# Performance work log

Measured on AMD Instinct MI355X. Metric: run time of the kernel, lower is better.

Reference implementation:

```python
import jax, jax.numpy as jnp
import numpy as np

B = 16
NT, NH_, NW_, T_, H_, W_ = 4, 14, 14, 4, 1, 1
C = 768
NHEAD = 12
HD = C // NHEAD
SCALE = 1.0 / float(np.sqrt(HD))
TT = NT * T_            # 16 temporal slices
T2 = TT // 2            # 8 after even/odd split
HW = (NH_ * H_) * (NW_ * W_)  # 196 spatial tokens
TOKENS = NT * NH_ * NW_ * T_ * H_ * W_


def setup_inputs() -> dict:
    key = jax.random.key(0)
    ks = jax.random.split(key, 14)
    def lin(k, din, dout):
        return jax.random.normal(k, (din, dout), jnp.float32) * 0.02
    return {
        "x_in": jax.random.normal(ks[0], (B, TOKENS, C), jnp.float32),
        "Wq_d": lin(ks[1], C, C),      "bq_d": jnp.zeros((C,), jnp.float32),
        "Wkv_a": lin(ks[2], C, 2 * C), "bkv_a": jnp.zeros((2 * C,), jnp.float32),
        "Wq_a": lin(ks[3], C, C),      "bq_a": jnp.zeros((C,), jnp.float32),
        "Wkv_d": lin(ks[4], C, 2 * C), "bkv_d": jnp.zeros((2 * C,), jnp.float32),
        "Wp_d": lin(ks[5], C, C),      "bp_d": jnp.zeros((C,), jnp.float32),
        "Wp_a": lin(ks[6], C, C),      "bp_a": jnp.zeros((C,), jnp.float32),
    }


def _cross_attn(q_x, kv_x, Wq, bq, Wkv, bkv):
    # q_x, kv_x: (b, t, hw, c)
    b, t, hw, c = q_x.shape
    q = (q_x @ Wq + bq).reshape(b, t, hw, NHEAD, HD)
    kv = (kv_x @ Wkv + bkv).reshape(b, t, hw, 2, NHEAD, HD)
    k, v = kv[..., 0, :, :], kv[..., 1, :, :]
    s = jnp.einsum('btqhd,btkhd->bthqk', q, k) * SCALE
    p = jax.nn.softmax(s, axis=-1)
    o = jnp.einsum('bthqk,btkhd->btqhd', p, v)
    return o.reshape(b, t, hw, c)


def reference(x_in, Wq_d, bq_d, Wkv_a, bkv_a, Wq_a, bq_a, Wkv_d, bkv_d,
              Wp_d, bp_d, Wp_a, bp_a):
    b = x_in.shape[0]
    # einops: b (nt nh nw t h w) c -> b (nt t) (nh h) (nw w) c
    x = x_in.reshape(b, NT, NH_, NW_, T_, H_, W_, C)
    x = x.transpose(0, 1, 4, 2, 5, 3, 6, 7).reshape(b, TT, NH_ * H_, NW_ * W_, C)
    x_skip = x                                   # (b, TT, h, w, c)
    x = x.reshape(b, TT, HW, C)                  # (b, TT, hw, c)
    x_a = x[:, 0::2]                             # (b, T2, hw, c) approx
    x_d = x[:, 1::2]                             # (b, T2, hw, c) detail

    # detail cross-attends to approx, subtract-update
    _d = _cross_attn(x_d, x_a, Wq_d, bq_d, Wkv_a, bkv_a)
    _d = jax.nn.gelu(_d @ Wp_d + bp_d, approximate=False)
    x_d = x_d - _d
    # approx cross-attends to updated detail, add-update
    _a = _cross_attn(x_a, x_d, Wq_a, bq_a, Wkv_d, bkv_d)
    _a = jax.nn.gelu(_a @ Wp_a + bp_a, approximate=False)
    x_a = x_a + _a

    # relaxed_constrain: pooled-skip minus channel-mean of x_a
    xs = x_skip.reshape(b, TT, HW, C)
    pooled = xs.reshape(b, T2, 2, HW, C).mean(axis=2)   # avg_pool2d (2,1)
    pool_a = pooled.mean(axis=-1) - x_a.mean(axis=-1)   # (b, T2, hw)

    # SSL=False: mean over channels, keepdim (torch layout b,1,t,hw)
    x_d_out = x_d.mean(axis=-1)[:, None, :, :]          # (b, 1, T2, hw)
    return (pool_a, x_d_out)
```

## Files before the change

### kernel.cpp

```cpp
#include <hip/hip_runtime.h>

typedef __bf16 bf16;
typedef __attribute__((ext_vector_type(8))) __bf16 bf16x8;
typedef __attribute__((ext_vector_type(4))) __bf16 bf16x4;
typedef __attribute__((ext_vector_type(2))) __bf16 bf16x2;
typedef __attribute__((ext_vector_type(4))) float f32x4;
typedef __attribute__((ext_vector_type(4))) unsigned int u32x4;

#define TOKENS 3136
#define CC 768
#define S196 196
#define M_ROWS 25088
#define BATCH 16

__device__ __forceinline__ float bf2f(bf16 x) { return (float)x; }
__device__ __forceinline__ bf16 f2bf(float x) { return (bf16)x; }

__device__ __forceinline__ float gelu_exact(float x) {
    return 0.5f * x * (1.0f + erff(x * 0.70710678118654752f));
}

__device__ __forceinline__ unsigned int packbf(float a, float b) {
    bf16x2 v; v[0] = (bf16)a; v[1] = (bf16)b;
    return __builtin_bit_cast(unsigned int, v);
}

#define GLOAD_LDS16(gp, lp) \
    __builtin_amdgcn_global_load_lds((const __attribute__((address_space(1))) void*)(gp), \
                                     (__attribute__((address_space(3))) void*)(lp), 16, 0, 0)

__global__ __launch_bounds__(256)
void transpose_all(const float* W0, const float* W1, const float* W2,
                   const float* W3, const float* W4, const float* W5,
                   bf16* D0, bf16* D1, bf16* D2, bf16* D3, bf16* D4, bf16* D5)
{
    const int base[7] = {0, 576, 1728, 2304, 3456, 4032, 4608};
    const float* srcs[6] = {W0, W1, W2, W3, W4, W5};
    bf16*        dsts[6] = {D0, D1, D2, D3, D4, D5};
    const int    Ns[6]   = {768, 1536, 768, 1536, 768, 768};

    int bid = blockIdx.x;
    int which = 0;
    #pragma unroll
    for (int j = 0; j < 6; ++j) if (bid >= base[j + 1]) which = j + 1;
    int t  = bid - base[which];
    int N  = Ns[which];
    const float* W  = srcs[which];
    bf16*        Wt = dsts[which];
    const int K = 768;

    int kx = t % 24, ny = t / 24;
    int k0 = kx * 32, n0 = ny * 32;

    __shared__ float tle[32][33];
    int tx = threadIdx.x & 31, ty = threadIdx.x >> 5;
    for (int r = ty; r < 32; r += 8)
        tle[r][tx] = W[(long)(k0 + r) * N + n0 + tx];
    __syncthreads();
    for (int r = ty; r < 32; r += 8)
        Wt[(long)(n0 + r) * K + k0 + tx] = f2bf(tle[tx][r]);
}

__global__ __launch_bounds__(256)
void conv_bias(const float* b0, const float* b1, const float* b2,
               const float* b3, const float* b4, const float* b5,
               bf16* __restrict__ dst)
{
    const float* srcs[6] = {b0, b1, b2, b3, b4, b5};
    const int sizes[6]   = {768, 1536, 768, 1536, 768, 768};
    const int offs[6]    = {0, 768, 2304, 3072, 4608, 5376};
    int which = blockIdx.x;
    const float* s = srcs[which];
    int n = sizes[which];
    bf16* d = dst + offs[which];
    for (int i = threadIdx.x; i < n; i += 256)
        d[i] = f2bf(s[i]);
}

__global__ __launch_bounds__(256)
void reorder_split(const float* __restrict__ x_in, bf16* __restrict__ xa,
                   bf16* __restrict__ xd)
{
    long idx = (long)blockIdx.x * 256 + threadIdx.x;
    const long total = (long)BATCH * 16 * S196 * 96;
    if (idx >= total) return;
    int  c8  = (int)(idx % 96) * 8;
    long row = idx / 96;
    int  s   = (int)(row % S196);
    long r2  = row / S196;
    int  tt  = (int)(r2 & 15);
    int  b   = (int)(r2 >> 4);
    int  nt  = tt >> 2, t = tt & 3;
    int  nh  = s / 14,  nw = s % 14;
    long src  = ((long)b * TOKENS + ((nt * 14 + nh) * 14 + nw) * 4 + t) * CC + c8;
    bf16* dst = (tt & 1) ? xd : xa;
    long doff = ((long)(b * 8 + (tt >> 1)) * S196 + s) * CC + c8;
    const float* sp = x_in + src;
    f32x4 a = *(const f32x4*)sp;
    f32x4 c = *(const f32x4*)(sp + 4);
    bf16x8 v;
    v[0] = f2bf(a[0]); v[1] = f2bf(a[1]); v[2] = f2bf(a[2]); v[3] = f2bf(a[3]);
    v[4] = f2bf(c[0]); v[5] = f2bf(c[1]); v[6] = f2bf(c[2]); v[7] = f2bf(c[3]);
    *(bf16x8*)(dst + doff) = v;
}

__device__ __forceinline__ float row_sum768(const bf16* __restrict__ p, int lane)
{
    float s = 0.f;
    bf16x8 v = *(const bf16x8*)(p + lane * 8);
    #pragma unroll
    for (int j = 0; j < 8; ++j) s += bf2f(v[j]);
    if (lane < 32) {
        bf16x8 w = *(const bf16x8*)(p + 512 + lane * 8);
        #pragma unroll
        for (int j = 0; j < 8; ++j) s += bf2f(w[j]);
    }
    #pragma unroll
    for (int off = 32; off; off >>= 1) s += __shfl_xor(s, off, 64);
    return s;
}

__global__ __launch_bounds__(256)
void pool_ad(const bf16* __restrict__ xa, const bf16* __restrict__ xd,
             float* __restrict__ pool0, float* __restrict__ rs_a,
             float* __restrict__ rs_d)
{
    int id = blockIdx.x * 4 + (threadIdx.x >> 6);
    int lane = threadIdx.x & 63;
    float sa = row_sum768(xa + (long)id * CC, lane);
    float sd = row_sum768(xd + (long)id * CC, lane);
    if (lane == 0) {
        pool0[id] = (sa + sd) * (0.5f / 768.0f);
        rs_a[id] = 0.f;
        rs_d[id] = 0.f;
    }
}

__global__ __launch_bounds__(256)
void out_combine(const float* __restrict__ pool0, const float* __restrict__ rs_a,
                 const float* __restrict__ rs_d, float* __restrict__ out)
{
    int id = blockIdx.x * 256 + threadIdx.x;
    if (id < M_ROWS) {
        out[id]          = pool0[id] - rs_a[id] * (1.0f / 768.0f);
        out[M_ROWS + id] = rs_d[id] * (1.0f / 768.0f);
    }
}

template<int EPI>
__global__ __launch_bounds__(256, 4)
void gemm_bt128(const bf16* __restrict__ A, const bf16* __restrict__ Bt,
                const bf16* __restrict__ bias, const bf16* __restrict__ res,
                bf16* __restrict__ C, float* __restrict__ rowsum,
                int ldc, int K, int mTiles, int nTiles)
{
    constexpr int BM = 128, BK = 32;
    __shared__ alignas(16) bf16 sA[BM * BK];
    __shared__ alignas(16) bf16 sB[BM * BK];
    const int tid  = threadIdx.x;
    const int lane = tid & 63, wave = tid >> 6;
    const int wm   = wave >> 1, wn = wave & 1;
    const int quad = lane >> 4, l16 = lane & 15;

    int nwg  = (int)gridDim.x;
    int orig = (int)blockIdx.x;
    int q8 = nwg >> 3, r8 = nwg & 7, xcd = orig & 7;
    int pid = (xcd < r8 ? xcd * (q8 + 1) : r8 * (q8 + 1) + (xcd - r8) * q8)
              + (orig >> 3);

    const int GM = 16;
    int group = GM * nTiles;
    int gid   = pid / group;
    int rem   = pid - gid * group;
    int first = gid * GM;
    int gm    = (mTiles - first < GM) ? (mTiles - first) : GM;
    int bm    = first + rem % gm;
    int bn    = rem / gm;

    const long m0 = (long)bm * BM;
    const long n0 = (long)bn * BM;

    f32x4 acc[4][4] = {};

    for (int kt = 0; kt < K; kt += BK) {
        if (kt) __syncthreads();
        #pragma unroll
        for (int c = 0; c < 2; ++c) {
            int ci = (wave * 2 + c) * 64 + lane;
            int r  = ci >> 2, kc = ci & 3;
            const bf16* ga = A  + (m0 + r) * K + kt + kc * 8;
            const bf16* gb = Bt + (n0 + r) * K + kt + kc * 8;
            bf16* la = sA + (wave * 2 + c) * 512;
            bf16* lb = sB + (wave * 2 + c) * 512;
            GLOAD_LDS16(ga, la);
            GLOAD_LDS16(gb, lb);
        }
        __syncthreads();

        bf16x8 af[4], bfr[4];
        #pragma unroll
        for (int mi = 0; mi < 4; ++mi)
            af[mi] = *(const bf16x8*)(sA + (wm * 64 + mi * 16 + l16) * BK + quad * 8);
        #pragma unroll
        for (int ni = 0; ni < 4; ++ni)
            bfr[ni] = *(const bf16x8*)(sB + (wn * 64 + ni * 16 + l16) * BK + quad * 8);
        #pragma unroll
        for (int mi = 0; mi < 4; ++mi)
            #pragma unroll
            for (int ni = 0; ni < 4; ++ni)
                acc[mi][ni] = __builtin_amdgcn_mfma_f32_16x16x32_bf16(af[mi], bfr[ni], acc[mi][ni], 0, 0, 0);
    }

    float bns[4];
    #pragma unroll
    for (int ni = 0; ni < 4; ++ni)
        bns[ni] = bf2f(bias[(int)n0 + wn * 64 + ni * 16 + l16]);

    #pragma unroll
    for (int mi = 0; mi < 4; ++mi) {
        float rs[4] = {0.f, 0.f, 0.f, 0.f};
        int mg = (int)m0 + wm * 64 + mi * 16 + quad * 4;
        #pragma unroll
        for (int ni = 0; ni < 4; ++ni) {
            int ng = (int)n0 + wn * 64 + ni * 16 + l16;
            #pragma unroll
            for (int r = 0; r < 4; ++r) {
                float x = acc[mi][ni][r] + bns[ni];
                long off = (long)(mg + r) * ldc + ng;
                if (EPI == 0) {
                    C[off] = f2bf(x);
                } else if (EPI == 1) {
                    bf16 v = f2bf(bf2f(res[off]) - gelu_exact(x));
                    C[off] = v;
                    rs[r] += bf2f(v);
                } else {
                    bf16 v = f2bf(bf2f(res[off]) + gelu_exact(x));
                    rs[r] += bf2f(v);
                }
            }
        }
        if (EPI != 0) {
            #pragma unroll
            for (int r = 0; r < 4; ++r) {
                float v = rs[r];
                v += __shfl_xor(v, 1, 64);
                v += __shfl_xor(v, 2, 64);
                v += __shfl_xor(v, 4, 64);
                v += __shfl_xor(v, 8, 64);
                if (l16 == 0)
                    atomicAdd(&rowsum[mg + r], v);
            }
        }
    }
}

template<int EPI>
__global__ __launch_bounds__(512, 2)
void gemm_bt256(const bf16* __restrict__ A, const bf16* __restrict__ Bt,
                const bf16* __restrict__ bias, const bf16* __restrict__ res,
                bf16* __restrict__ C, int ldc, int mTiles, int nTiles)
{
    constexpr int K = 768, NKT = 12;
    __shared__ alignas(16) bf16 sA[4][8192];
    __shared__ alignas(16) bf16 sB[4][8192];
    const int tid  = threadIdx.x;
    const int lane = tid & 63, wave = tid >> 6;
    const int wm   = wave >> 2, wn = wave & 3;
    const int quad = lane >> 4, l16 = lane & 15;

    int nwg  = (int)gridDim.x;
    int orig = (int)blockIdx.x;
    int q8 = nwg >> 3, r8 = nwg & 7, xcd = orig & 7;
    int pid = (xcd < r8 ? xcd * (q8 + 1) : r8 * (q8 + 1) + (xcd - r8) * q8)
              + (orig >> 3);

    const int GM = 8;
    int group = GM * nTiles;
    int gid   = pid / group;
    int rem   = pid - gid * group;
    int first = gid * GM;
    int gm    = (mTiles - first < GM) ? (mTiles - first) : GM;
    int bm    = first + rem % gm;
    int bn    = rem / gm;

    const long m0 = (long)bm * 256;
    const long n0 = (long)bn * 256;

    const int lh  = l16 >> 1;
    const int px  = ((l16 & 1) << 2) | quad;
    const int pxl = (px ^ lh) * 8;
    const int aoffA = (wm * 64 + lh) * 64 + pxl;
    const int aoffB = (wn * 32 + lh) * 64 + pxl;

    const int  cg  = (tid & 7) ^ ((tid >> 3) & 7);
    const int  rr  = ((tid >> 3) << 1) + (cg >> 2);
    const long soA0 = (long)rr * K + (cg & 3) * 8;
    const long soA1 = (long)(128 + rr) * K + (cg & 3) * 8;
    const int  ldd0 = wave * 512, ldd1 = 4096 + wave * 512;
    const bf16* Ab = A  + m0 * K;
    const bf16* Bb = Bt + n0 * K;

    f32x4 acc[8][4] = {};

    #define STG_A(slot, koff) do { \
        GLOAD_LDS16(Ab + (koff) + soA0, &sA[slot][ldd0]); \
        GLOAD_LDS16(Ab + (koff) + soA1, &sA[slot][ldd1]); } while (0)
    #define STG_B(slot, koff) do { \
        GLOAD_LDS16(Bb + (koff) + soA0, &sB[slot][ldd0]); \
        GLOAD_LDS16(Bb + (koff) + soA1, &sB[slot][ldd1]); } while (0)

    STG_A(0, 0);  STG_B(0, 0);
    STG_A(1, 32); STG_B(1, 32);
    STG_A(2, 64); STG_B(2, 64);
    asm volatile("s_waitcnt vmcnt(8)" ::: "memory");
    __builtin_amdgcn_s_barrier();

    #define MFMA16(H) do { \
        __builtin_amdgcn_s_setprio(1); \
        _Pragma("unroll") \
        for (int mf = 0; mf < 4; ++mf) \
            _Pragma("unroll") \
            for (int nf = 0; nf < 4; ++nf) \
                acc[(H)*4 + mf][nf] = __builtin_amdgcn_mfma_f32_16x16x32_bf16( \
                    a[mf], b[nf], acc[(H)*4 + mf][nf], 0, 0, 0); \
        __builtin_amdgcn_s_setprio(0); } while (0)

    #pragma unroll 2
    for (int t = 0; t < NKT; ++t) {
        const int sl0 = (2 * t) & 3;
        const int sl1 = (2 * t + 1) & 3;
        const int slN = (2 * t + 3) & 3;
        bf16x8 a[4], b[4];

        #pragma unroll
        for (int mf = 0; mf < 4; ++mf) a[mf] = *(const bf16x8*)(&sA[sl0][mf * 512 + aoffA]);
        #pragma unroll
        for (int nf = 0; nf < 4; ++nf) b[nf] = *(const bf16x8*)(&sB[sl0][nf * 512 + aoffB]);
        if (t + 1 < NKT) STG_A(slN, (t + 1) * 64 + 32);
        __builtin_amdgcn_s_barrier();
        MFMA16(0);
        __builtin_amdgcn_s_barrier();

        #pragma unroll
        for (int mf = 0; mf < 4; ++mf) a[mf] = *(const bf16x8*)(&sA[sl0][2048 + mf * 512 + aoffA]);
        if (t + 1 < NKT) STG_B(slN, (t + 1) * 64 + 32);
        __builtin_amdgcn_s_barrier();
        MFMA16(1);
        if (t + 1 < NKT) asm volatile("s_waitcnt vmcnt(8)" ::: "memory");
        else             asm volatile("s_waitcnt vmcnt(0)" ::: "memory");
        __builtin_amdgcn_s_barrier();

        #pragma unroll
        for (int mf = 0; mf < 4; ++mf) a[mf] = *(const bf16x8*)(&sA[sl1][mf * 512 + aoffA]);
        #pragma unroll
        for (int nf = 0; nf < 4; ++nf) b[nf] = *(const bf16x8*)(&sB[sl1][nf * 512 + aoffB]);
        if (t + 2 < NKT) STG_A(sl0, (t + 2) * 64);
        __builtin_amdgcn_s_barrier();
        MFMA16(0);
        __builtin_amdgcn_s_barrier();

        #pragma unroll
        for (int mf = 0; mf < 4; ++mf) a[mf] = *(const bf16x8*)(&sA[sl1][2048 + mf * 512 + aoffA]);
        if (t + 2 < NKT) STG_B(sl0, (t + 2) * 64);
        __builtin_amdgcn_s_barrier();
        MFMA16(1);
        if      (t + 2 < NKT) asm volatile("s_waitcnt vmcnt(8)" ::: "memory");
        else if (t + 1 < NKT) asm volatile("s_waitcnt vmcnt(4)" ::: "memory");
        __builtin_amdgcn_s_barrier();
    }
    #undef STG_A
    #undef STG_B
    #undef MFMA16

    #pragma unroll
    for (int mf = 0; mf < 8; ++mf) {
        #pragma unroll
        for (int nf = 0; nf < 4; ++nf) {
            int mg = (int)m0 + wm * 128 + mf * 16 + quad * 4;
            int ng = (int)n0 + wn * 64 + nf * 16 + l16;
            float bn_ = bf2f(bias[ng]);
            #pragma unroll
            for (int r = 0; r < 4; ++r) {
                float x = acc[mf][nf][r] + bn_;
                long off = (long)(mg + r) * ldc + ng;
                if (EPI == 0)      C[off] = f2bf(x);
                else if (EPI == 1) C[off] = f2bf(bf2f(res[off]) - gelu_exact(x));
                else               C[off] = f2bf(bf2f(res[off]) + gelu_exact(x));
            }
        }
    }
}

#define KSTR 72
#define VSTR 264

__global__ __launch_bounds__(256)
void attn_mfma(const bf16* __restrict__ Q, int ldq,
               const bf16* __restrict__ KV, int ldkv,
               bf16* __restrict__ O)
{
    const int h  = blockIdx.x;
    const int bj = blockIdx.y;
    __shared__ alignas(16) bf16 Ks[208 * KSTR];
    __shared__ alignas(16) bf16 Vt[64 * VSTR];
    const int tid = threadIdx.x, lane = tid & 63, wave = tid >> 6;
    const int quad = lane >> 4, l16 = lane & 15;

    const bf16* qg = Q  + (long)bj * S196 * ldq  + h * 64;
    const bf16* kg = KV + (long)bj * S196 * ldkv + h * 64;
    const bf16* vg = kg + CC;

    for (int i = tid; i < 208 * 8; i += 256) {
        int r = i >> 3, c8 = (i & 7) * 8;
        bf16x8 v = {};
        if (r < S196) v = *(const bf16x8*)(kg + (long)r * ldkv + c8);
        *(bf16x8*)(Ks + r * KSTR + c8) = v;
    }
    for (int i = tid; i < 256 * 8; i += 256) {
        int g   = i >> 6;
        int c8  = (g & 7) * 8;
        int tok = (g >> 3) * 64 + (i & 63);
        bf16x8 v = {};
        if (tok < S196) v = *(const bf16x8*)(vg + (long)tok * ldkv + c8);
        #pragma unroll
        for (int j = 0; j < 8; ++j)
            Vt[(c8 + j) * VSTR + tok] = v[j];
    }
    __syncthreads();

    for (int qt = wave; qt < 13; qt += 4) {
        int qrow = qt * 16 + l16; if (qrow > 195) qrow = 195;
        const bf16* qrp = qg + (long)qrow * ldq + quad * 8;
        bf16x8 qf0 = *(const bf16x8*)(qrp);
        bf16x8 qf1 = *(const bf16x8*)(qrp + 32);

        f32x4 st[13];
        #pragma unroll
        for (int rt = 0; rt < 13; ++rt) st[rt] = (f32x4){0.f, 0.f, 0.f, 0.f};
        #pragma unroll
        for (int rt = 0; rt < 13; ++rt) {
            const bf16* kb = Ks + (rt * 16 + l16) * KSTR + quad * 8;
            bf16x8 kf0 = *(const bf16x8*)(kb);
            bf16x8 kf1 = *(const bf16x8*)(kb + 32);
            st[rt] = __builtin_amdgcn_mfma_f32_16x16x32_bf16(kf0, qf0, st[rt], 0, 0, 0);
            st[rt] = __builtin_amdgcn_mfma_f32_16x16x32_bf16(kf1, qf1, st[rt], 0, 0, 0);
        }

        const float SC = 0.125f;
        #pragma unroll
        for (int rt = 0; rt < 13; ++rt) {
            st[rt][0] *= SC; st[rt][1] *= SC; st[rt][2] *= SC; st[rt][3] *= SC;
        }
        if (quad != 0)
            st[12] = (f32x4){-1e30f, -1e30f, -1e30f, -1e30f};

        float m = -1e30f;
        #pragma unroll
        for (int rt = 0; rt < 13; ++rt)
            m = fmaxf(m, fmaxf(fmaxf(st[rt][0], st[rt][1]), fmaxf(st[rt][2], st[rt][3])));
        m = fmaxf(m, __shfl_xor(m, 16, 64));
        m = fmaxf(m, __shfl_xor(m, 32, 64));
        float sum = 0.f;
        #pragma unroll
        for (int rt = 0; rt < 13; ++rt) {
            st[rt][0] = __expf(st[rt][0] - m);
            st[rt][1] = __expf(st[rt][1] - m);
            st[rt][2] = __expf(st[rt][2] - m);
            st[rt][3] = __expf(st[rt][3] - m);
            sum += st[rt][0] + st[rt][1] + st[rt][2] + st[rt][3];
        }
        sum += __shfl_xor(sum, 16, 64);
        sum += __shfl_xor(sum, 32, 64);
        float inv = 1.0f / sum;

        unsigned int pk[13][2];
        #pragma unroll
        for (int rt = 0; rt < 13; ++rt) {
            pk[rt][0] = packbf(st[rt][0] * inv, st[rt][1] * inv);
            pk[rt][1] = packbf(st[rt][2] * inv, st[rt][3] * inv);
        }

        f32x4 ot[4];
        #pragma unroll
        for (int dt = 0; dt < 4; ++dt) ot[dt] = (f32x4){0.f, 0.f, 0.f, 0.f};
        #pragma unroll
        for (int c = 0; c < 7; ++c) {
            u32x4 fp;
            #pragma unroll
            for (int jp = 0; jp < 4; ++jp) {
                int jh = jp >> 1, rp = jp & 1;
                int srcb = ((((quad & 1) << 1) + jh) << 6) | (l16 << 2);
                int a = __builtin_amdgcn_ds_bpermute(srcb, (int)pk[2 * c][rp]);
                int b = (c < 6) ? __builtin_amdgcn_ds_bpermute(srcb, (int)pk[2 * c + 1][rp]) : 0;
                fp[jp] = (quad >> 1) ? (unsigned int)b : (unsigned int)a;
            }
            bf16x8 pB = __builtin_bit_cast(bf16x8, fp);
            #pragma unroll
            for (int dt = 0; dt < 4; ++dt) {
                bf16x8 vf = *(const bf16x8*)(Vt + (dt * 16 + l16) * VSTR + c * 32 + quad * 8);
                ot[dt] = __builtin_amdgcn_mfma_f32_16x16x32_bf16(vf, pB, ot[dt], 0, 0, 0);
            }
        }

        int token = qt * 16 + l16;
        if (token < S196) {
            bf16* op = O + ((long)bj * S196 + token) * CC + h * 64 + quad * 4;
            #pragma unroll
            for (int dt = 0; dt < 4; ++dt) {
                bf16x4 v;
                v[0] = f2bf(ot[dt][0]); v[1] = f2bf(ot[dt][1]);
                v[2] = f2bf(ot[dt][2]); v[3] = f2bf(ot[dt][3]);
                *(bf16x4*)(op + dt * 16) = v;
            }
        }
    }
}

extern "C" void kernel_launch(void* const* d_in, const int* in_sizes, int n_in,
                              void* d_out, int out_size, void* d_ws, size_t ws_size,
                              hipStream_t stream)
{
    const float* x_in  = (const float*)d_in[0];
    const float* Wq_d  = (const float*)d_in[1];
    const float* bq_d  = (const float*)d_in[2];
    const float* Wkv_a = (const float*)d_in[3];
    const float* bkv_a = (const float*)d_in[4];
    const float* Wq_a  = (const float*)d_in[5];
    const float* bq_a  = (const float*)d_in[6];
    const float* Wkv_d = (const float*)d_in[7];
    const float* bkv_d = (const float*)d_in[8];
    const float* Wp_d  = (const float*)d_in[9];
    const float* bp_d  = (const float*)d_in[10];
    const float* Wp_a  = (const float*)d_in[11];
    const float* bp_a  = (const float*)d_in[12];
    float* out = (float*)d_out;

    char* w = (char*)d_ws;
    auto alloc = [&](size_t elems) {
        bf16* p = (bf16*)w;
        w += ((elems * 2 + 255) / 256) * 256;
        return p;
    };
    bf16* biasAll = alloc(6144);
    bf16* WtQd  = alloc((size_t)768 * 768);
    bf16* WtACat= alloc((size_t)2304 * 768);
    bf16* WtKd  = alloc((size_t)1536 * 768);
    bf16* WtPd  = alloc((size_t)768 * 768);
    bf16* WtPa  = alloc((size_t)768 * 768);
    bf16* xa    = alloc((size_t)M_ROWS * 768);
    bf16* xd    = alloc((size_t)M_ROWS * 768);
    bf16* Qb    = alloc((size_t)M_ROWS * 768);
    bf16* QKVa  = alloc((size_t)M_ROWS * 2304);
    bf16* Ob    = alloc((size_t)M_ROWS * 768);
    float* pool0 = (float*)w; w += ((size_t)M_ROWS * 4 + 255) / 256 * 256;
    float* rs_a  = (float*)w; w += ((size_t)M_ROWS * 4 + 255) / 256 * 256;
    float* rs_d  = (float*)w; w += ((size_t)M_ROWS * 4 + 255) / 256 * 256;

    dim3 blk(256);
    dim3 blk512(512);

    transpose_all<<<dim3(4608), blk, 0, stream>>>(
        Wq_d, Wkv_a, Wq_a, Wkv_d, Wp_d, Wp_a,
        WtQd, WtACat, WtACat + (size_t)1536 * 768, WtKd, WtPd, WtPa);
    conv_bias<<<dim3(6), blk, 0, stream>>>(bq_d, bkv_a, bq_a, bkv_d, bp_d, bp_a, biasAll);

    long total_chunks = (long)BATCH * 16 * S196 * 96;
    int  rblocks = (int)((total_chunks + 255) / 256);
    reorder_split<<<rblocks, blk, 0, stream>>>(x_in, xa, xd);
    pool_ad<<<M_ROWS / 4, blk, 0, stream>>>(xa, xd, pool0, rs_a, rs_d);

    const bf16* Bq_d   = biasAll;
    const bf16* Bkva_qa= biasAll + 768;
    const bf16* Bkv_d  = biasAll + 3072;
    const bf16* Bp_d   = biasAll + 4608;
    const bf16* Bp_a   = biasAll + 5376;

    gemm_bt128<0><<<dim3(196 * 6), blk, 0, stream>>>(xd, WtQd, Bq_d, nullptr, Qb, nullptr, 768, 768, 196, 6);
    gemm_bt256<0><<<dim3(98 * 9), blk512, 0, stream>>>(xa, WtACat, Bkva_qa, nullptr, QKVa, 2304, 98, 9);
    attn_mfma<<<dim3(12, 128), blk, 0, stream>>>(Qb, 768, QKVa, 2304, Ob);
    gemm_bt128<1><<<dim3(196 * 6), blk, 0, stream>>>(Ob, WtPd, Bp_d, xd, xd, rs_d, 768, 768, 196, 6);

    gemm_bt128<0><<<dim3(196 * 12), blk, 0, stream>>>(xd, WtKd, Bkv_d, nullptr, QKVa, nullptr, 2304, 768, 196, 12);
    attn_mfma<<<dim3(12, 128), blk, 0, stream>>>(QKVa + 1536, 2304, QKVa, 2304, Ob);
    gemm_bt128<2><<<dim3(196 * 6), blk, 0, stream>>>(Ob, WtPa, Bp_a, xa, nullptr, rs_a, 768, 768, 196, 6);

    out_combine<<<dim3((M_ROWS + 255) / 256), blk, 0, stream>>>(pool0, rs_a, rs_d, out);
}
```

Before: 843.9 us.

## Fuse prep kernels, fold pooling into reorder, use 256-tile GEMM for KV

Merges the weight transpose, bias conversion and zeroing of the pool/rowsum buffers into a single prep kernel. Drops the separate pool_ad pass by computing the skip-pool row sums inside reorder_split with wave reductions and atomicAdd, which avoids re-reading xa/xd. Switches the detail KV projection to the larger 256-tile GEMM. The changes trade fewer launches and less memory traffic for atomic contention and summation over fp32 inputs in a different order.

```diff
diff --git a/kernel.cpp b/kernel.cpp
--- a/kernel.cpp
+++ b/kernel.cpp
@@ -30,60 +30,57 @@
                                      (__attribute__((address_space(3))) void*)(lp), 16, 0, 0)
 
 __global__ __launch_bounds__(256)
-void transpose_all(const float* W0, const float* W1, const float* W2,
-                   const float* W3, const float* W4, const float* W5,
-                   bf16* D0, bf16* D1, bf16* D2, bf16* D3, bf16* D4, bf16* D5)
-{
-    const int base[7] = {0, 576, 1728, 2304, 3456, 4032, 4608};
-    const float* srcs[6] = {W0, W1, W2, W3, W4, W5};
-    bf16*        dsts[6] = {D0, D1, D2, D3, D4, D5};
-    const int    Ns[6]   = {768, 1536, 768, 1536, 768, 768};
-
+void prep_all(const float* W0, const float* W1, const float* W2,
+              const float* W3, const float* W4, const float* W5,
+              const float* b0, const float* b1, const float* b2,
+              const float* b3, const float* b4, const float* b5,
+              bf16* D0, bf16* D1, bf16* D2, bf16* D3, bf16* D4, bf16* D5,
+              bf16* __restrict__ biasAll, float* __restrict__ zbase)
+{
     int bid = blockIdx.x;
-    int which = 0;
-    #pragma unroll
-    for (int j = 0; j < 6; ++j) if (bid >= base[j + 1]) which = j + 1;
-    int t  = bid - base[which];
-    int N  = Ns[which];
-    const float* W  = srcs[which];
-    bf16*        Wt = dsts[which];
-    const int K = 768;
-
-    int kx = t % 24, ny = t / 24;
-    int k0 = kx * 32, n0 = ny * 32;
-
-    __shared__ float tle[32][33];
-    int tx = threadIdx.x & 31, ty = threadIdx.x >> 5;
-    for (int r = ty; r < 32; r += 8)
-        tle[r][tx] = W[(long)(k0 + r) * N + n0 + tx];
-    __syncthreads();
-    for (int r = ty; r < 32; r += 8)
-        Wt[(long)(n0 + r) * K + k0 + tx] = f2bf(tle[tx][r]);
-}
-
-__global__ __launch_bounds__(256)
-void conv_bias(const float* b0, const float* b1, const float* b2,
-               const float* b3, const float* b4, const float* b5,
-               bf16* __restrict__ dst)
-{
-    const float* srcs[6] = {b0, b1, b2, b3, b4, b5};
-    const int sizes[6]   = {768, 1536, 768, 1536, 768, 768};
-    const int offs[6]    = {0, 768, 2304, 3072, 4608, 5376};
-    int which = blockIdx.x;
-    const float* s = srcs[which];
-    int n = sizes[which];
-    bf16* d = dst + offs[which];
-    for (int i = threadIdx.x; i < n; i += 256)
-        d[i] = f2bf(s[i]);
+    int tid = threadIdx.x;
+    if (bid < 4608) {
+        const int base[7] = {0, 576, 1728, 2304, 3456, 4032, 4608};
+        const float* srcs[6] = {W0, W1, W2, W3, W4, W5};
+        bf16*        dsts[6] = {D0, D1, D2, D3, D4, D5};
+        const int    Ns[6]   = {768, 1536, 768, 1536, 768, 768};
+        int which = 0;
+        #pragma unroll
+        for (int j = 0; j < 6; ++j) if (bid >= base[j + 1]) which = j + 1;
+        int t  = bid - base[which];
+        int N  = Ns[which];
+        const float* W  = srcs[which];
+        bf16*        Wt = dsts[which];
+        const int K = 768;
+        int kx = t % 24, ny = t / 24;
+        int k0 = kx * 32, n0 = ny * 32;
+        __shared__ float tle[32][33];
+        int tx = tid & 31, ty = tid >> 5;
+        for (int r = ty; r < 32; r += 8)
+            tle[r][tx] = W[(long)(k0 + r) * N + n0 + tx];
+        __syncthreads();
+        for (int r = ty; r < 32; r += 8)
+            Wt[(long)(n0 + r) * K + k0 + tx] = f2bf(tle[tx][r]);
+    } else if (bid < 4614) {
+        const float* srcs[6] = {b0, b1, b2, b3, b4, b5};
+        const int sizes[6]   = {768, 1536, 768, 1536, 768, 768};
+        const int offs[6]    = {0, 768, 2304, 3072, 4608, 5376};
+        int which = bid - 4608;
+        const float* s = srcs[which];
+        int n = sizes[which];
+        bf16* d = biasAll + offs[which];
+        for (int i = tid; i < n; i += 256)
+            d[i] = f2bf(s[i]);
+    } else {
+        zbase[(bid - 4614) * 256 + tid] = 0.f;
+    }
 }
 
 __global__ __launch_bounds__(256)
 void reorder_split(const float* __restrict__ x_in, bf16* __restrict__ xa,
-                   bf16* __restrict__ xd)
+                   bf16* __restrict__ xd, float* __restrict__ pool0)
 {
     long idx = (long)blockIdx.x * 256 + threadIdx.x;
-    const long total = (long)BATCH * 16 * S196 * 96;
-    if (idx >= total) return;
     int  c8  = (int)(idx % 96) * 8;
     long row = idx / 96;
     int  s   = (int)(row % S196);
@@ -94,7 +91,8 @@
     int  nh  = s / 14,  nw = s % 14;
     long src  = ((long)b * TOKENS + ((nt * 14 + nh) * 14 + nw) * 4 + t) * CC + c8;
     bf16* dst = (tt & 1) ? xd : xa;
-    long doff = ((long)(b * 8 + (tt >> 1)) * S196 + s) * CC + c8;
+    int  id   = (b * 8 + (tt >> 1)) * S196 + s;
+    long doff = (long)id * CC + c8;
     const float* sp = x_in + src;
     f32x4 a = *(const f32x4*)sp;
     f32x4 c = *(const f32x4*)(sp + 4);
@@ -102,38 +100,19 @@
     v[0] = f2bf(a[0]); v[1] = f2bf(a[1]); v[2] = f2bf(a[2]); v[3] = f2bf(a[3]);
     v[4] = f2bf(c[0]); v[5] = f2bf(c[1]); v[6] = f2bf(c[2]); v[7] = f2bf(c[3]);
     *(bf16x8*)(dst + doff) = v;
-}
-
-__device__ __forceinline__ float row_sum768(const bf16* __restrict__ p, int lane)
-{
-    float s = 0.f;
-    bf16x8 v = *(const bf16x8*)(p + lane * 8);
+
+    float ssum = a[0] + a[1] + a[2] + a[3] + c[0] + c[1] + c[2] + c[3];
+    int lane = threadIdx.x & 63;
+    int id0  = __shfl(id, 0, 64);
+    float s1 = (id == id0) ? ssum : 0.f;
+    float s2 = ssum - s1;
     #pragma unroll
-    for (int j = 0; j < 8; ++j) s += bf2f(v[j]);
-    if (lane < 32) {
-        bf16x8 w = *(const bf16x8*)(p + 512 + lane * 8);
-        #pragma unroll
-        for (int j = 0; j < 8; ++j) s += bf2f(w[j]);
-    }
-    #pragma unroll
-    for (int off = 32; off; off >>= 1) s += __shfl_xor(s, off, 64);
-    return s;
-}
-
-__global__ __launch_bounds__(256)
-void pool_ad(const bf16* __restrict__ xa, const bf16* __restrict__ xd,
-             float* __restrict__ pool0, float* __restrict__ rs_a,
-             float* __restrict__ rs_d)
-{
-    int id = blockIdx.x * 4 + (threadIdx.x >> 6);
-    int lane = threadIdx.x & 63;
-    float sa = row_sum768(xa + (long)id * CC, lane);
-    float sd = row_sum768(xd + (long)id * CC, lane);
-    if (lane == 0) {
-        pool0[id] = (sa + sd) * (0.5f / 768.0f);
-        rs_a[id] = 0.f;
-        rs_d[id] = 0.f;
-    }
+    for (int off = 32; off; off >>= 1) {
+        s1 += __shfl_xor(s1, off, 64);
+        s2 += __shfl_xor(s2, off, 64);
+    }
+    if (lane == 0) atomicAdd(&pool0[id0], s1 * (0.5f / 768.0f));
+    if (lane == 63 && id != id0) atomicAdd(&pool0[id], s2 * (0.5f / 768.0f));
 }
 
 __global__ __launch_bounds__(256)
@@ -559,15 +538,13 @@
     dim3 blk(256);
     dim3 blk512(512);
 
-    transpose_all<<<dim3(4608), blk, 0, stream>>>(
+    prep_all<<<dim3(4908), blk, 0, stream>>>(
         Wq_d, Wkv_a, Wq_a, Wkv_d, Wp_d, Wp_a,
-        WtQd, WtACat, WtACat + (size_t)1536 * 768, WtKd, WtPd, WtPa);
-    conv_bias<<<dim3(6), blk, 0, stream>>>(bq_d, bkv_a, bq_a, bkv_d, bp_d, bp_a, biasAll);
-
-    long total_chunks = (long)BATCH * 16 * S196 * 96;
-    int  rblocks = (int)((total_chunks + 255) / 256);
-    reorder_split<<<rblocks, blk, 0, stream>>>(x_in, xa, xd);
-    pool_ad<<<M_ROWS / 4, blk, 0, stream>>>(xa, xd, pool0, rs_a, rs_d);
+        bq_d, bkv_a, bq_a, bkv_d, bp_d, bp_a,
+        WtQd, WtACat, WtACat + (size_t)1536 * 768, WtKd, WtPd, WtPa,
+        biasAll, pool0);
+
+    reorder_split<<<dim3(18816), blk, 0, stream>>>(x_in, xa, xd, pool0);
 
     const bf16* Bq_d   = biasAll;
     const bf16* Bkva_qa= biasAll + 768;
@@ -580,7 +557,7 @@
     attn_mfma<<<dim3(12, 128), blk, 0, stream>>>(Qb, 768, QKVa, 2304, Ob);
     gemm_bt128<1><<<dim3(196 * 6), blk, 0, stream>>>(Ob, WtPd, Bp_d, xd, xd, rs_d, 768, 768, 196, 6);
 
-    gemm_bt128<0><<<dim3(196 * 12), blk, 0, stream>>>(xd, WtKd, Bkv_d, nullptr, QKVa, nullptr, 2304, 768, 196, 12);
+    gemm_bt256<0><<<dim3(98 * 6), blk512, 0, stream>>>(xd, WtKd, Bkv_d, nullptr, QKVa, 2304, 98, 6);
     attn_mfma<<<dim3(12, 128), blk, 0, stream>>>(QKVa + 1536, 2304, QKVa, 2304, Ob);
     gemm_bt128<2><<<dim3(196 * 6), blk, 0, stream>>>(Ob, WtPa, Bp_a, xa, nullptr, rs_a, 768, 768, 196, 6);
 
```

New measurement: 835.2 us. Within noise of the previous version (-1.0%).
